# Optimization experiments

Hardware: AMD Instinct MI355X
Metric: run time of the kernel (lower is better)

The kernel has to match this reference:

```python
import jax, jax.numpy as jnp
import numpy as np

D_MODEL = 1024
NUM_HEADS = 16
WINDOW = 128
DEPTH = D_MODEL // NUM_HEADS


def setup_inputs() -> dict:
    key = jax.random.key(0)
    ks = jax.random.split(key, 9)
    B, S = 2, 2048
    scale = 1.0 / np.sqrt(D_MODEL)
    x = jax.random.normal(ks[0], (B, S, D_MODEL), dtype=jnp.float32)
    Wq = jax.random.normal(ks[1], (D_MODEL, D_MODEL), dtype=jnp.float32) * scale
    Wk = jax.random.normal(ks[2], (D_MODEL, D_MODEL), dtype=jnp.float32) * scale
    Wv = jax.random.normal(ks[3], (D_MODEL, D_MODEL), dtype=jnp.float32) * scale
    Wo = jax.random.normal(ks[4], (D_MODEL, D_MODEL), dtype=jnp.float32) * scale
    bq = jnp.zeros((D_MODEL,), jnp.float32)
    bk = jnp.zeros((D_MODEL,), jnp.float32)
    bv = jnp.zeros((D_MODEL,), jnp.float32)
    bo = jnp.zeros((D_MODEL,), jnp.float32)
    return {"x": x, "Wq": Wq, "bq": bq, "Wk": Wk, "bk": bk,
            "Wv": Wv, "bv": bv, "Wo": Wo, "bo": bo}


def _split_heads(t, B, S):
    # [B,S,D] -> [B,H,S,depth]
    return t.reshape(B, S, NUM_HEADS, DEPTH).transpose(0, 2, 1, 3)


def reference(x, Wq, bq, Wk, bk, Wv, bv, Wo, bo):
    B, S, _ = x.shape
    q = _split_heads(x @ Wq + bq, B, S)
    k = _split_heads(x @ Wk + bk, B, S)
    v = _split_heads(x @ Wv + bv, B, S)
    scores = jnp.einsum('bhqd,bhkd->bhqk', q, k) / jnp.sqrt(jnp.float32(DEPTH))
    idx = jnp.arange(S)
    # mask[i_row=j, i_col=i] per original: |i - j| <= window (symmetric)
    local = jnp.abs(idx[None, :] - idx[:, None]) <= WINDOW  # [S,S]
    scores = jnp.where(local[None, None], scores, jnp.float32(-1e9))
    attn = jax.nn.softmax(scores, axis=-1)
    out = jnp.einsum('bhqk,bhkd->bhqd', attn, v)
    concat = out.transpose(0, 2, 1, 3).reshape(B, S, D_MODEL)
    return concat @ Wo + bo
```

## Files before the change

### kernel.cpp

```cpp
#include <hip/hip_runtime.h>
#include <cstdint>
#include <cstddef>

typedef __attribute__((ext_vector_type(8))) short short8;
typedef __attribute__((ext_vector_type(4))) short short4v;
typedef __attribute__((ext_vector_type(4))) float f32x4;
typedef short8 bf16x8;

typedef __attribute__((address_space(1))) const unsigned GU;
typedef __attribute__((address_space(3))) unsigned LU;

__device__ __forceinline__ short f2bf(float f) {
  unsigned u = __builtin_bit_cast(unsigned, f);
  u += 0x7fffu + ((u >> 16) & 1u);
  return (short)(u >> 16);
}

__global__ __launch_bounds__(256) void k_cast_x(const float* __restrict__ x, short* __restrict__ xb) {
  size_t i = ((size_t)blockIdx.x * 256 + threadIdx.x) * 8;
  f32x4 a = *(const f32x4*)(x + i);
  f32x4 b = *(const f32x4*)(x + i + 4);
  short8 o;
#pragma unroll
  for (int j = 0; j < 4; ++j) { o[j] = f2bf(a[j]); o[4 + j] = f2bf(b[j]); }
  *(short8*)(xb + i) = o;
}

__global__ __launch_bounds__(256) void k_tw(const float* __restrict__ W0, const float* __restrict__ W1,
                                            const float* __restrict__ W2, const float* __restrict__ W3,
                                            short* __restrict__ WT) {
  __shared__ short T[64 * 72];
  int bid = blockIdx.x;
  int widx = bid >> 8;
  int t = bid & 255;
  int kr = (t >> 4) * 64, nc = (t & 15) * 64;
  const float* W = widx == 0 ? W0 : widx == 1 ? W1 : widx == 2 ? W2 : W3;
  short* out = WT + (size_t)widx * 1048576;
  int tid = threadIdx.x;
#pragma unroll
  for (int i = 0; i < 4; ++i) {
    int idx = tid + i * 256;
    int k = idx >> 4, n4 = (idx & 15) << 2;
    f32x4 v = *(const f32x4*)(W + (size_t)(kr + k) * 1024 + nc + n4);
#pragma unroll
    for (int j = 0; j < 4; ++j) T[(n4 + j) * 72 + k] = f2bf(v[j]);
  }
  __syncthreads();
#pragma unroll
  for (int i = 0; i < 2; ++i) {
    int idx = tid + i * 256;
    int n = idx >> 3, k8 = (idx & 7) << 3;
    *(short8*)(out + (size_t)(nc + n) * 1024 + kr + k8) = *(const short8*)&T[n * 72 + k8];
  }
}

__global__ __launch_bounds__(256) void k_tv(const short* __restrict__ v, short* __restrict__ vT) {
  __shared__ short T[64 * 72];
  int bid = blockIdx.x;
  int stile = bid & 31, h = (bid >> 5) & 15, b = bid >> 9;
  int s0 = stile * 64;
  int tid = threadIdx.x;
#pragma unroll
  for (int i = 0; i < 2; ++i) {
    int idx = tid + i * 256;
    int s = idx >> 3, d0 = (idx & 7) << 3;
    short8 vec = *(const short8*)(v + ((size_t)b * 2048 + s0 + s) * 1024 + h * 64 + d0);
#pragma unroll
    for (int j = 0; j < 8; ++j) T[(d0 + j) * 72 + s] = vec[j];
  }
  __syncthreads();
#pragma unroll
  for (int i = 0; i < 2; ++i) {
    int idx = tid + i * 256;
    int d = idx >> 3, s8 = (idx & 7) << 3;
    *(short8*)(vT + (((size_t)b * 16 + h) * 64 + d) * 2048 + s0 + s8) = *(const short8*)&T[d * 72 + s8];
  }
}

template <int MODE>
__global__ __launch_bounds__(256, 2) void k_gemm(
    const short* __restrict__ A, const short* __restrict__ BT,
    const float* __restrict__ bias0, const float* __restrict__ bias1, const float* __restrict__ bias2,
    short* __restrict__ outb, float* __restrict__ outf) {
  __shared__ short Smem[16384];
  const int tid = threadIdx.x;
  const int lane = tid & 63, w = tid >> 6;
  const int g = lane >> 4, qi = lane & 15;
  const int wr = (w >> 1) * 64, wc = (w & 1) * 64;
  const int m0 = blockIdx.y * 128, n0 = blockIdx.x * 128;
  const size_t K = 1024;
  const short* Ab = A + (size_t)m0 * K;
  const short* Bb = BT + (size_t)n0 * K;

  auto stage = [&](int buf, int k0) {
    short* Asb = Smem + buf * 4096;
    short* Bsb = Smem + 8192 + buf * 4096;
#pragma unroll
    for (int i = 0; i < 2; ++i) {
      int cidx = tid + i * 256;
      int r = cidx >> 2;
      int csw = ((cidx & 3) ^ ((r >> 1) & 3)) << 3;
      __builtin_amdgcn_global_load_lds((GU*)(Ab + (size_t)r * K + k0 + csw),
                                       (LU*)(&Asb[cidx * 8]), 16, 0, 0);
      __builtin_amdgcn_global_load_lds((GU*)(Bb + (size_t)r * K + k0 + csw),
                                       (LU*)(&Bsb[cidx * 8]), 16, 0, 0);
    }
  };

  f32x4 acc[4][4];
#pragma unroll
  for (int i = 0; i < 4; ++i)
#pragma unroll
    for (int j = 0; j < 4; ++j) acc[i][j] = (f32x4)(0.0f);

  stage(0, 0);
  __syncthreads();
  for (int kt = 0; kt < 32; ++kt) {
    int cur = kt & 1;
    if (kt < 31) stage(cur ^ 1, (kt + 1) * 32);
    const short* Asb = Smem + cur * 4096;
    const short* Bsb = Smem + 8192 + cur * 4096;
    bf16x8 a[4], b[4];
#pragma unroll
    for (int mf = 0; mf < 4; ++mf) {
      int R = wr + mf * 16 + qi;
      a[mf] = *(const bf16x8*)&Asb[R * 32 + ((g ^ ((R >> 1) & 3)) << 3)];
    }
#pragma unroll
    for (int nf = 0; nf < 4; ++nf) {
      int R = wc + nf * 16 + qi;
      b[nf] = *(const bf16x8*)&Bsb[R * 32 + ((g ^ ((R >> 1) & 3)) << 3)];
    }
#pragma unroll
    for (int mf = 0; mf < 4; ++mf)
#pragma unroll
      for (int nf = 0; nf < 4; ++nf)
        acc[mf][nf] = __builtin_amdgcn_mfma_f32_16x16x32_bf16(a[mf], b[nf], acc[mf][nf], 0, 0, 0);
    __syncthreads();
  }

  if (MODE == 0) {
    int sel = n0 >> 10;
    const float* bias = sel == 0 ? bias0 : (sel == 1 ? bias1 : bias2);
    size_t outoff = (size_t)sel * 4194304;
    int ncol0 = n0 & 1023;
    float bv[4];
#pragma unroll
    for (int nf = 0; nf < 4; ++nf) bv[nf] = bias[ncol0 + wc + nf * 16 + qi];
    short* Os = Smem;
#pragma unroll
    for (int mf = 0; mf < 4; ++mf) {
      __syncthreads();
#pragma unroll
      for (int nf = 0; nf < 4; ++nf)
#pragma unroll
        for (int j = 0; j < 4; ++j)
          Os[((w >> 1) * 16 + g * 4 + j) * 136 + wc + nf * 16 + qi] = f2bf(acc[mf][nf][j] + bv[nf]);
      __syncthreads();
#pragma unroll
      for (int i = 0; i < 2; ++i) {
        int idx = tid + i * 256;
        int r = idx >> 4, c8 = (idx & 15) << 3;
        int row = m0 + ((r >> 4) << 6) + mf * 16 + (r & 15);
        *(short8*)&outb[outoff + (size_t)row * 1024 + ncol0 + c8] = *(const short8*)&Os[r * 136 + c8];
      }
    }
  } else {
    float* Ft = (float*)Smem;
    float bv[4];
#pragma unroll
    for (int nf = 0; nf < 4; ++nf) bv[nf] = bias0[n0 + wc + nf * 16 + qi];
#pragma unroll
    for (int mf = 0; mf < 4; ++mf) {
      __syncthreads();
#pragma unroll
      for (int nf = 0; nf < 4; ++nf)
#pragma unroll
        for (int j = 0; j < 4; ++j)
          Ft[((w >> 1) * 16 + g * 4 + j) * 136 + wc + nf * 16 + qi] = acc[mf][nf][j] + bv[nf];
      __syncthreads();
#pragma unroll
      for (int i = 0; i < 4; ++i) {
        int idx = tid + i * 256;
        int r = idx >> 5, c4 = (idx & 31) << 2;
        int row = m0 + ((r >> 4) << 6) + mf * 16 + (r & 15);
        *(f32x4*)&outf[(size_t)row * 1024 + n0 + c4] = *(const f32x4*)&Ft[r * 136 + c4];
      }
    }
  }
}

__global__ __launch_bounds__(256, 2) void k_attn(const short* __restrict__ qg_,
                                                 const short* __restrict__ kg_,
                                                 const short* __restrict__ vT,
                                                 short* __restrict__ outp) {
  __shared__ short Qs[64 * 72];
  __shared__ short Ks[64 * 72];
  __shared__ short Vs[64 * 72];
  __shared__ short Ps[4][16 * 72];
  int bid = blockIdx.x;
  int qt = bid & 31, h = (bid >> 5) & 15, b = bid >> 9;
  int q0 = qt * 64;
  int tid = threadIdx.x, lane = tid & 63, w = tid >> 6;
  int g = lane >> 4, qi = lane & 15;

  const short* qsrc = qg_ + ((size_t)b * 2048 + q0) * 1024 + h * 64;
#pragma unroll
  for (int i = 0; i < 2; ++i) {
    int idx = tid + i * 256;
    int r = idx >> 3, c = (idx & 7) << 3;
    *(short8*)&Qs[r * 72 + c] = *(const short8*)&qsrc[(size_t)r * 1024 + c];
  }

  float m = -1e30f, l = 0.f;
  f32x4 oacc[4];
#pragma unroll
  for (int i = 0; i < 4; ++i) oacc[i] = (f32x4)(0.0f);
  int qglob = q0 + w * 16 + qi;

  for (int cc = 0; cc < 5; ++cc) {
    int kb0 = q0 - 128 + cc * 64;
    if (kb0 < 0 || kb0 >= 2048) continue;
    __syncthreads();
    const short* ksrc = kg_ + ((size_t)b * 2048 + kb0) * 1024 + h * 64;
    const short* vsrc = vT + ((size_t)(b * 16 + h)) * 64 * 2048 + kb0;
#pragma unroll
    for (int i = 0; i < 2; ++i) {
      int idx = tid + i * 256;
      int r = idx >> 3, c = (idx & 7) << 3;
      *(short8*)&Ks[r * 72 + c] = *(const short8*)&ksrc[(size_t)r * 1024 + c];
      *(short8*)&Vs[r * 72 + c] = *(const short8*)&vsrc[(size_t)r * 2048 + c];
    }
    __syncthreads();

    f32x4 st[4];
#pragma unroll
    for (int i = 0; i < 4; ++i) st[i] = (f32x4)(0.0f);
#pragma unroll
    for (int ds = 0; ds < 2; ++ds) {
      bf16x8 qf = *(const bf16x8*)&Qs[(w * 16 + qi) * 72 + ds * 32 + g * 8];
#pragma unroll
      for (int mf = 0; mf < 4; ++mf) {
        bf16x8 kf = *(const bf16x8*)&Ks[(mf * 16 + qi) * 72 + ds * 32 + g * 8];
        st[mf] = __builtin_amdgcn_mfma_f32_16x16x32_bf16(kf, qf, st[mf], 0, 0, 0);
      }
    }

    float pv[16];
    float pm = -1e30f;
#pragma unroll
    for (int mf = 0; mf < 4; ++mf)
#pragma unroll
      for (int j = 0; j < 4; ++j) {
        int kcol = kb0 + mf * 16 + g * 4 + j;
        float s = st[mf][j] * 0.125f;
        int d = kcol - qglob;
        bool valid = (d >= -128) && (d <= 128);
        s = valid ? s : -1e30f;
        pv[mf * 4 + j] = s;
        pm = fmaxf(pm, s);
      }
    pm = fmaxf(pm, __shfl_xor(pm, 16));
    pm = fmaxf(pm, __shfl_xor(pm, 32));
    float mnew = fmaxf(m, pm);
    float scale = __expf(m - mnew);
    float ls = 0.f;
#pragma unroll
    for (int e = 0; e < 16; ++e) {
      float p = pv[e] > -1e29f ? __expf(pv[e] - mnew) : 0.f;
      pv[e] = p;
      ls += p;
    }
    ls += __shfl_xor(ls, 16);
    ls += __shfl_xor(ls, 32);
    l = l * scale + ls;
    m = mnew;
#pragma unroll
    for (int mf = 0; mf < 4; ++mf) oacc[mf] *= scale;

#pragma unroll
    for (int f = 0; f < 4; ++f) {
      short4v pk;
#pragma unroll
      for (int j = 0; j < 4; ++j) pk[j] = f2bf(pv[f * 4 + j]);
      *(short4v*)&Ps[w][qi * 72 + f * 16 + g * 4] = pk;
    }

#pragma unroll
    for (int ks = 0; ks < 2; ++ks) {
      bf16x8 pf = *(const bf16x8*)&Ps[w][qi * 72 + ks * 32 + g * 8];
#pragma unroll
      for (int mf = 0; mf < 4; ++mf) {
        bf16x8 vf = *(const bf16x8*)&Vs[(mf * 16 + qi) * 72 + ks * 32 + g * 8];
        oacc[mf] = __builtin_amdgcn_mfma_f32_16x16x32_bf16(vf, pf, oacc[mf], 0, 0, 0);
      }
    }
  }

  __syncthreads();
  short* Os = Ks;
  float inv = 1.f / l;
#pragma unroll
  for (int mf = 0; mf < 4; ++mf) {
    short4v pk;
#pragma unroll
    for (int j = 0; j < 4; ++j) pk[j] = f2bf(oacc[mf][j] * inv);
    *(short4v*)&Os[(w * 16 + qi) * 72 + mf * 16 + g * 4] = pk;
  }
  __syncthreads();
  short* dst = outp + ((size_t)b * 2048 + q0) * 1024 + h * 64;
  int r = tid >> 2, c16 = (tid & 3) << 4;
  *(short8*)&dst[(size_t)r * 1024 + c16] = *(const short8*)&Os[r * 72 + c16];
  *(short8*)&dst[(size_t)r * 1024 + c16 + 8] = *(const short8*)&Os[r * 72 + c16 + 8];
}

extern "C" void kernel_launch(void* const* d_in, const int* in_sizes, int n_in,
                              void* d_out, int out_size, void* d_ws, size_t ws_size,
                              hipStream_t stream) {
  const float* x  = (const float*)d_in[0];
  const float* Wq = (const float*)d_in[1];
  const float* bq = (const float*)d_in[2];
  const float* Wk = (const float*)d_in[3];
  const float* bk = (const float*)d_in[4];
  const float* Wv = (const float*)d_in[5];
  const float* bv = (const float*)d_in[6];
  const float* Wo = (const float*)d_in[7];
  const float* bo = (const float*)d_in[8];

  short* ws = (short*)d_ws;
  short* xb       = ws;
  short* qkv      = ws + 4194304;
  short* vbuf     = qkv + 2 * 4194304;
  short* vT       = ws;
  short* attn_out = vbuf;
  short* WT       = ws + 4 * 4194304;

  k_cast_x<<<2048, 256, 0, stream>>>(x, xb);
  k_tw<<<1024, 256, 0, stream>>>(Wq, Wk, Wv, Wo, WT);
  {
    dim3 grid(24, 32);
    k_gemm<0><<<grid, 256, 0, stream>>>(xb, WT, bq, bk, bv, qkv, nullptr);
  }
  k_tv<<<1024, 256, 0, stream>>>(vbuf, vT);
  k_attn<<<1024, 256, 0, stream>>>(qkv, qkv + 4194304, vT, attn_out);
  {
    dim3 grid(8, 32);
    k_gemm<1><<<grid, 256, 0, stream>>>(attn_out, WT + 3 * 1048576, bo, bo, bo, nullptr, (float*)d_out);
  }
}
```

Measured before the change: 96.34 us.

## Replace QKV GEMM with 256x256-tile, 8-wave, multi-stage pipelined kernel

The fused QKV projection GEMM moves from 128x128 tiles with 4 waves to 256x256 tiles with 8 waves. Global-to-LDS loads are staged in half-k chunks across a 128KB LDS ring and interleaved with MFMA phases, using explicit barriers, waitcnt and setprio. A block-index swizzle is added to improve L2 reuse. The larger tile cuts operand reloads and is meant to hide memory latency, but the grid drops to 192 blocks on 256 CUs, so some CUs sit idle.

Result: faster. 92.98 us (-3.5%).

```diff
diff --git a/kernel.cpp b/kernel.cpp
--- a/kernel.cpp
+++ b/kernel.cpp
@@ -77,11 +77,134 @@
   }
 }
 
-template <int MODE>
-__global__ __launch_bounds__(256, 2) void k_gemm(
+__global__ __launch_bounds__(512, 2) void k_gemm256(
     const short* __restrict__ A, const short* __restrict__ BT,
     const float* __restrict__ bias0, const float* __restrict__ bias1, const float* __restrict__ bias2,
-    short* __restrict__ outb, float* __restrict__ outf) {
+    short* __restrict__ outb) {
+  __shared__ short S[65536];
+  const int tid = threadIdx.x;
+  const int lane = tid & 63, w = tid >> 6;
+  const int g = lane >> 4, qi = lane & 15;
+  const int wm = w >> 2, wn = w & 3;
+  int bid = blockIdx.x;
+  int swz = (bid & 7) * 24 + (bid >> 3);
+  const int tm = swz / 12, tn = swz % 12;
+  const int m0 = tm * 256, n0 = tn * 256;
+  const size_t K = 1024;
+  const short* Ab = A + (size_t)m0 * K;
+  const short* Bb = BT + (size_t)n0 * K;
+
+  auto stage = [&](int roff, const short* gbase, int kt, int kh) {
+    int k0 = kt * 64 + kh * 32;
+#pragma unroll
+    for (int i = 0; i < 2; ++i) {
+      int c = tid + i * 512;
+      int r = c >> 2;
+      int csw = ((c & 3) ^ ((r >> 1) & 3)) << 3;
+      __builtin_amdgcn_global_load_lds((GU*)(gbase + (size_t)r * K + k0 + csw),
+                                       (LU*)(&S[roff + c * 8]), 16, 0, 0);
+    }
+  };
+  auto lda = [&](int roff, int row) -> bf16x8 {
+    return *(const bf16x8*)&S[roff + row * 32 + ((g ^ ((row >> 1) & 3)) << 3)];
+  };
+
+  f32x4 acc[8][4];
+#pragma unroll
+  for (int i = 0; i < 8; ++i)
+#pragma unroll
+    for (int j = 0; j < 4; ++j) acc[i][j] = (f32x4)(0.0f);
+
+#define MF1(rh, mf, nf, av, bv) \
+  acc[(rh)*4+(mf)][(nf)] = __builtin_amdgcn_mfma_f32_16x16x32_bf16(av, bv, acc[(rh)*4+(mf)][(nf)], 0, 0, 0)
+
+#define GPH(buf, kh, rh, ...) do { \
+    const int ra_ = (buf)*32768 + (kh)*8192; \
+    const int rb_ = (buf)*32768 + 16384 + (kh)*8192; \
+    const int ar_ = wm*128 + (rh)*64 + qi; \
+    bf16x8 a0 = lda(ra_, ar_ + 0);  bf16x8 a1 = lda(ra_, ar_ + 16); \
+    bf16x8 a2 = lda(ra_, ar_ + 32); bf16x8 a3 = lda(ra_, ar_ + 48); \
+    const int br_ = wn*64 + qi; \
+    bf16x8 b0 = lda(rb_, br_ + 0);  bf16x8 b1 = lda(rb_, br_ + 16); \
+    bf16x8 b2 = lda(rb_, br_ + 32); bf16x8 b3 = lda(rb_, br_ + 48); \
+    __VA_ARGS__; \
+    __builtin_amdgcn_sched_barrier(0); \
+    __builtin_amdgcn_s_barrier(); \
+    asm volatile("s_waitcnt lgkmcnt(0)" ::: "memory"); \
+    __builtin_amdgcn_sched_barrier(0); \
+    __builtin_amdgcn_s_setprio(1); \
+    MF1(rh,0,0,a0,b0); MF1(rh,0,1,a0,b1); MF1(rh,0,2,a0,b2); MF1(rh,0,3,a0,b3); \
+    MF1(rh,1,0,a1,b0); MF1(rh,1,1,a1,b1); MF1(rh,1,2,a1,b2); MF1(rh,1,3,a1,b3); \
+    MF1(rh,2,0,a2,b0); MF1(rh,2,1,a2,b1); MF1(rh,2,2,a2,b2); MF1(rh,2,3,a2,b3); \
+    MF1(rh,3,0,a3,b0); MF1(rh,3,1,a3,b1); MF1(rh,3,2,a3,b2); MF1(rh,3,3,a3,b3); \
+    __builtin_amdgcn_s_setprio(0); \
+    __builtin_amdgcn_sched_barrier(0); \
+  } while (0)
+
+  stage(0,     Ab, 0, 0);
+  stage(16384, Bb, 0, 0);
+  stage(8192,  Ab, 0, 1);
+  stage(24576, Bb, 0, 1);
+  stage(32768, Ab, 1, 0);
+  stage(49152, Bb, 1, 0);
+  asm volatile("s_waitcnt vmcnt(4)" ::: "memory");
+  __builtin_amdgcn_s_barrier();
+
+  for (int j = 0; j < 8; ++j) {
+    int t1 = 2 * j + 1;
+    int t2 = 2 * j + 2; t2 = t2 < 15 ? t2 : 15;
+    int t3 = 2 * j + 3; t3 = t3 < 15 ? t3 : 15;
+    GPH(0, 0, 0, stage(40960, Ab, t1, 1));  __builtin_amdgcn_s_barrier();
+    GPH(0, 0, 1, stage(57344, Bb, t1, 1));  __builtin_amdgcn_s_barrier();
+    GPH(0, 1, 0, stage(0,     Ab, t2, 0));  __builtin_amdgcn_s_barrier();
+    GPH(0, 1, 1, stage(16384, Bb, t2, 0));
+      asm volatile("s_waitcnt vmcnt(4)" ::: "memory");
+      __builtin_amdgcn_s_barrier();
+    GPH(1, 0, 0, stage(8192,  Ab, t2, 1));  __builtin_amdgcn_s_barrier();
+    GPH(1, 0, 1, stage(24576, Bb, t2, 1));  __builtin_amdgcn_s_barrier();
+    GPH(1, 1, 0, stage(32768, Ab, t3, 0));  __builtin_amdgcn_s_barrier();
+    GPH(1, 1, 1, stage(49152, Bb, t3, 0));
+      asm volatile("s_waitcnt vmcnt(4)" ::: "memory");
+      __builtin_amdgcn_s_barrier();
+  }
+#undef GPH
+#undef MF1
+
+  asm volatile("s_waitcnt vmcnt(0)" ::: "memory");
+  __syncthreads();
+  int sel = n0 >> 10;
+  const float* bias = sel == 0 ? bias0 : (sel == 1 ? bias1 : bias2);
+  size_t outoff = (size_t)sel * 4194304;
+  int ncol0 = n0 & 1023;
+  float bv[4];
+#pragma unroll
+  for (int nf = 0; nf < 4; ++nf) bv[nf] = bias[ncol0 + wn * 64 + nf * 16 + qi];
+  short* Ep = S;
+#pragma unroll
+  for (int rh = 0; rh < 2; ++rh) {
+    __syncthreads();
+#pragma unroll
+    for (int mf = 0; mf < 4; ++mf)
+#pragma unroll
+      for (int nf = 0; nf < 4; ++nf)
+#pragma unroll
+        for (int j = 0; j < 4; ++j)
+          Ep[(wm * 64 + mf * 16 + g * 4 + j) * 264 + wn * 64 + nf * 16 + qi] =
+              f2bf(acc[rh * 4 + mf][nf][j] + bv[nf]);
+    __syncthreads();
+#pragma unroll
+    for (int i = 0; i < 8; ++i) {
+      int idx = tid + i * 512;
+      int r = idx >> 5, c8 = (idx & 31) << 3;
+      int grow = m0 + (r >> 6) * 128 + rh * 64 + (r & 63);
+      *(short8*)&outb[outoff + (size_t)grow * 1024 + ncol0 + c8] = *(const short8*)&Ep[r * 264 + c8];
+    }
+  }
+}
+
+__global__ __launch_bounds__(256, 2) void k_gemmO(
+    const short* __restrict__ A, const short* __restrict__ BT,
+    const float* __restrict__ bias0, float* __restrict__ outf) {
   __shared__ short Smem[16384];
   const int tid = threadIdx.x;
   const int lane = tid & 63, w = tid >> 6;
@@ -139,53 +262,25 @@
     __syncthreads();
   }
 
-  if (MODE == 0) {
-    int sel = n0 >> 10;
-    const float* bias = sel == 0 ? bias0 : (sel == 1 ? bias1 : bias2);
-    size_t outoff = (size_t)sel * 4194304;
-    int ncol0 = n0 & 1023;
-    float bv[4];
-#pragma unroll
-    for (int nf = 0; nf < 4; ++nf) bv[nf] = bias[ncol0 + wc + nf * 16 + qi];
-    short* Os = Smem;
-#pragma unroll
-    for (int mf = 0; mf < 4; ++mf) {
-      __syncthreads();
-#pragma unroll
-      for (int nf = 0; nf < 4; ++nf)
-#pragma unroll
-        for (int j = 0; j < 4; ++j)
-          Os[((w >> 1) * 16 + g * 4 + j) * 136 + wc + nf * 16 + qi] = f2bf(acc[mf][nf][j] + bv[nf]);
-      __syncthreads();
-#pragma unroll
-      for (int i = 0; i < 2; ++i) {
-        int idx = tid + i * 256;
-        int r = idx >> 4, c8 = (idx & 15) << 3;
-        int row = m0 + ((r >> 4) << 6) + mf * 16 + (r & 15);
-        *(short8*)&outb[outoff + (size_t)row * 1024 + ncol0 + c8] = *(const short8*)&Os[r * 136 + c8];
-      }
-    }
-  } else {
-    float* Ft = (float*)Smem;
-    float bv[4];
-#pragma unroll
-    for (int nf = 0; nf < 4; ++nf) bv[nf] = bias0[n0 + wc + nf * 16 + qi];
-#pragma unroll
-    for (int mf = 0; mf < 4; ++mf) {
-      __syncthreads();
-#pragma unroll
-      for (int nf = 0; nf < 4; ++nf)
-#pragma unroll
-        for (int j = 0; j < 4; ++j)
-          Ft[((w >> 1) * 16 + g * 4 + j) * 136 + wc + nf * 16 + qi] = acc[mf][nf][j] + bv[nf];
-      __syncthreads();
-#pragma unroll
-      for (int i = 0; i < 4; ++i) {
-        int idx = tid + i * 256;
-        int r = idx >> 5, c4 = (idx & 31) << 2;
-        int row = m0 + ((r >> 4) << 6) + mf * 16 + (r & 15);
-        *(f32x4*)&outf[(size_t)row * 1024 + n0 + c4] = *(const f32x4*)&Ft[r * 136 + c4];
-      }
+  float* Ft = (float*)Smem;
+  float bv[4];
+#pragma unroll
+  for (int nf = 0; nf < 4; ++nf) bv[nf] = bias0[n0 + wc + nf * 16 + qi];
+#pragma unroll
+  for (int mf = 0; mf < 4; ++mf) {
+    __syncthreads();
+#pragma unroll
+    for (int nf = 0; nf < 4; ++nf)
+#pragma unroll
+      for (int j = 0; j < 4; ++j)
+        Ft[((w >> 1) * 16 + g * 4 + j) * 136 + wc + nf * 16 + qi] = acc[mf][nf][j] + bv[nf];
+    __syncthreads();
+#pragma unroll
+    for (int i = 0; i < 4; ++i) {
+      int idx = tid + i * 256;
+      int r = idx >> 5, c4 = (idx & 31) << 2;
+      int row = m0 + ((r >> 4) << 6) + mf * 16 + (r & 15);
+      *(f32x4*)&outf[(size_t)row * 1024 + n0 + c4] = *(const f32x4*)&Ft[r * 136 + c4];
     }
   }
 }
@@ -337,14 +432,11 @@
 
   k_cast_x<<<2048, 256, 0, stream>>>(x, xb);
   k_tw<<<1024, 256, 0, stream>>>(Wq, Wk, Wv, Wo, WT);
-  {
-    dim3 grid(24, 32);
-    k_gemm<0><<<grid, 256, 0, stream>>>(xb, WT, bq, bk, bv, qkv, nullptr);
-  }
+  k_gemm256<<<192, 512, 0, stream>>>(xb, WT, bq, bk, bv, qkv);
   k_tv<<<1024, 256, 0, stream>>>(vbuf, vT);
   k_attn<<<1024, 256, 0, stream>>>(qkv, qkv + 4194304, vT, attn_out);
   {
     dim3 grid(8, 32);
-    k_gemm<1><<<grid, 256, 0, stream>>>(attn_out, WT + 3 * 1048576, bo, bo, bo, nullptr, (float*)d_out);
-  }
-}
+    k_gemmO<<<grid, 256, 0, stream>>>(attn_out, WT + 3 * 1048576, bo, (float*)d_out);
+  }
+}
```

## Merge prep kernels, drop V transpose kernel, remap QKV GEMM tiles per XCD

Applied to the files above, without the earlier changes.

Merges the x cast and weight transpose into one launch. Removes the separate V transpose kernel: attention now reads V in its original layout and transposes it into LDS with a rotated column swizzle, so the MFMA read side changes to match. The QKV GEMM becomes a 1D grid whose block index is remapped so each XCD works on a contiguous group of M and N tiles, aiming for better L2 reuse. Together these cut two launches and one full pass over V through global memory, at the cost of scalar LDS stores of V inside attention.

Result: faster. 86.35 us (-10.4%).

```diff
diff --git a/kernel.cpp b/kernel.cpp
--- a/kernel.cpp
+++ b/kernel.cpp
@@ -16,27 +16,29 @@
   return (short)(u >> 16);
 }
 
-__global__ __launch_bounds__(256) void k_cast_x(const float* __restrict__ x, short* __restrict__ xb) {
-  size_t i = ((size_t)blockIdx.x * 256 + threadIdx.x) * 8;
-  f32x4 a = *(const f32x4*)(x + i);
-  f32x4 b = *(const f32x4*)(x + i + 4);
-  short8 o;
-#pragma unroll
-  for (int j = 0; j < 4; ++j) { o[j] = f2bf(a[j]); o[4 + j] = f2bf(b[j]); }
-  *(short8*)(xb + i) = o;
-}
-
-__global__ __launch_bounds__(256) void k_tw(const float* __restrict__ W0, const float* __restrict__ W1,
-                                            const float* __restrict__ W2, const float* __restrict__ W3,
-                                            short* __restrict__ WT) {
+__global__ __launch_bounds__(256) void k_prep(const float* __restrict__ x,
+                                              const float* __restrict__ W0, const float* __restrict__ W1,
+                                              const float* __restrict__ W2, const float* __restrict__ W3,
+                                              short* __restrict__ xb, short* __restrict__ WT) {
   __shared__ short T[64 * 72];
   int bid = blockIdx.x;
+  int tid = threadIdx.x;
+  if (bid < 2048) {
+    size_t i = ((size_t)bid * 256 + tid) * 8;
+    f32x4 a = *(const f32x4*)(x + i);
+    f32x4 b = *(const f32x4*)(x + i + 4);
+    short8 o;
+#pragma unroll
+    for (int j = 0; j < 4; ++j) { o[j] = f2bf(a[j]); o[4 + j] = f2bf(b[j]); }
+    *(short8*)(xb + i) = o;
+    return;
+  }
+  bid -= 2048;
   int widx = bid >> 8;
   int t = bid & 255;
   int kr = (t >> 4) * 64, nc = (t & 15) * 64;
   const float* W = widx == 0 ? W0 : widx == 1 ? W1 : widx == 2 ? W2 : W3;
   short* out = WT + (size_t)widx * 1048576;
-  int tid = threadIdx.x;
 #pragma unroll
   for (int i = 0; i < 4; ++i) {
     int idx = tid + i * 256;
@@ -54,34 +56,101 @@
   }
 }
 
-__global__ __launch_bounds__(256) void k_tv(const short* __restrict__ v, short* __restrict__ vT) {
-  __shared__ short T[64 * 72];
-  int bid = blockIdx.x;
-  int stile = bid & 31, h = (bid >> 5) & 15, b = bid >> 9;
-  int s0 = stile * 64;
-  int tid = threadIdx.x;
-#pragma unroll
-  for (int i = 0; i < 2; ++i) {
-    int idx = tid + i * 256;
-    int s = idx >> 3, d0 = (idx & 7) << 3;
-    short8 vec = *(const short8*)(v + ((size_t)b * 2048 + s0 + s) * 1024 + h * 64 + d0);
-#pragma unroll
-    for (int j = 0; j < 8; ++j) T[(d0 + j) * 72 + s] = vec[j];
-  }
-  __syncthreads();
-#pragma unroll
-  for (int i = 0; i < 2; ++i) {
-    int idx = tid + i * 256;
-    int d = idx >> 3, s8 = (idx & 7) << 3;
-    *(short8*)(vT + (((size_t)b * 16 + h) * 64 + d) * 2048 + s0 + s8) = *(const short8*)&T[d * 72 + s8];
-  }
-}
-
-template <int MODE>
-__global__ __launch_bounds__(256, 2) void k_gemm(
+__global__ __launch_bounds__(256, 2) void k_gemmQKV(
     const short* __restrict__ A, const short* __restrict__ BT,
     const float* __restrict__ bias0, const float* __restrict__ bias1, const float* __restrict__ bias2,
-    short* __restrict__ outb, float* __restrict__ outf) {
+    short* __restrict__ outb) {
+  __shared__ short Smem[16384];
+  const int tid = threadIdx.x;
+  const int lane = tid & 63, w = tid >> 6;
+  const int g = lane >> 4, qi = lane & 15;
+  const int wr = (w >> 1) * 64, wc = (w & 1) * 64;
+  int bid = blockIdx.x;
+  int xcd = bid & 7, ii = bid >> 3;
+  const int tm = (xcd >> 1) * 8 + ii / 12;
+  const int tn = (xcd & 1) * 12 + ii % 12;
+  const int m0 = tm * 128, n0 = tn * 128;
+  const size_t K = 1024;
+  const short* Ab = A + (size_t)m0 * K;
+  const short* Bb = BT + (size_t)n0 * K;
+
+  auto stage = [&](int buf, int k0) {
+    short* Asb = Smem + buf * 4096;
+    short* Bsb = Smem + 8192 + buf * 4096;
+#pragma unroll
+    for (int i = 0; i < 2; ++i) {
+      int cidx = tid + i * 256;
+      int r = cidx >> 2;
+      int csw = ((cidx & 3) ^ ((r >> 1) & 3)) << 3;
+      __builtin_amdgcn_global_load_lds((GU*)(Ab + (size_t)r * K + k0 + csw),
+                                       (LU*)(&Asb[cidx * 8]), 16, 0, 0);
+      __builtin_amdgcn_global_load_lds((GU*)(Bb + (size_t)r * K + k0 + csw),
+                                       (LU*)(&Bsb[cidx * 8]), 16, 0, 0);
+    }
+  };
+
+  f32x4 acc[4][4];
+#pragma unroll
+  for (int i = 0; i < 4; ++i)
+#pragma unroll
+    for (int j = 0; j < 4; ++j) acc[i][j] = (f32x4)(0.0f);
+
+  stage(0, 0);
+  __syncthreads();
+  for (int kt = 0; kt < 32; ++kt) {
+    int cur = kt & 1;
+    if (kt < 31) stage(cur ^ 1, (kt + 1) * 32);
+    const short* Asb = Smem + cur * 4096;
+    const short* Bsb = Smem + 8192 + cur * 4096;
+    bf16x8 a[4], b[4];
+#pragma unroll
+    for (int mf = 0; mf < 4; ++mf) {
+      int R = wr + mf * 16 + qi;
+      a[mf] = *(const bf16x8*)&Asb[R * 32 + ((g ^ ((R >> 1) & 3)) << 3)];
+    }
+#pragma unroll
+    for (int nf = 0; nf < 4; ++nf) {
+      int R = wc + nf * 16 + qi;
+      b[nf] = *(const bf16x8*)&Bsb[R * 32 + ((g ^ ((R >> 1) & 3)) << 3)];
+    }
+#pragma unroll
+    for (int mf = 0; mf < 4; ++mf)
+#pragma unroll
+      for (int nf = 0; nf < 4; ++nf)
+        acc[mf][nf] = __builtin_amdgcn_mfma_f32_16x16x32_bf16(a[mf], b[nf], acc[mf][nf], 0, 0, 0);
+    __syncthreads();
+  }
+
+  int sel = n0 >> 10;
+  const float* bias = sel == 0 ? bias0 : (sel == 1 ? bias1 : bias2);
+  size_t outoff = (size_t)sel * 4194304;
+  int ncol0 = n0 & 1023;
+  float bv[4];
+#pragma unroll
+  for (int nf = 0; nf < 4; ++nf) bv[nf] = bias[ncol0 + wc + nf * 16 + qi];
+  short* Os = Smem;
+#pragma unroll
+  for (int mf = 0; mf < 4; ++mf) {
+    __syncthreads();
+#pragma unroll
+    for (int nf = 0; nf < 4; ++nf)
+#pragma unroll
+      for (int j = 0; j < 4; ++j)
+        Os[((w >> 1) * 16 + g * 4 + j) * 136 + wc + nf * 16 + qi] = f2bf(acc[mf][nf][j] + bv[nf]);
+    __syncthreads();
+#pragma unroll
+    for (int i = 0; i < 2; ++i) {
+      int idx = tid + i * 256;
+      int r = idx >> 4, c8 = (idx & 15) << 3;
+      int row = m0 + ((r >> 4) << 6) + mf * 16 + (r & 15);
+      *(short8*)&outb[outoff + (size_t)row * 1024 + ncol0 + c8] = *(const short8*)&Os[r * 136 + c8];
+    }
+  }
+}
+
+__global__ __launch_bounds__(256, 2) void k_gemmO(
+    const short* __restrict__ A, const short* __restrict__ BT,
+    const float* __restrict__ bias0, float* __restrict__ outf) {
   __shared__ short Smem[16384];
   const int tid = threadIdx.x;
   const int lane = tid & 63, w = tid >> 6;
@@ -139,60 +208,32 @@
     __syncthreads();
   }
 
-  if (MODE == 0) {
-    int sel = n0 >> 10;
-    const float* bias = sel == 0 ? bias0 : (sel == 1 ? bias1 : bias2);
-    size_t outoff = (size_t)sel * 4194304;
-    int ncol0 = n0 & 1023;
-    float bv[4];
-#pragma unroll
-    for (int nf = 0; nf < 4; ++nf) bv[nf] = bias[ncol0 + wc + nf * 16 + qi];
-    short* Os = Smem;
-#pragma unroll
-    for (int mf = 0; mf < 4; ++mf) {
-      __syncthreads();
-#pragma unroll
-      for (int nf = 0; nf < 4; ++nf)
-#pragma unroll
-        for (int j = 0; j < 4; ++j)
-          Os[((w >> 1) * 16 + g * 4 + j) * 136 + wc + nf * 16 + qi] = f2bf(acc[mf][nf][j] + bv[nf]);
-      __syncthreads();
-#pragma unroll
-      for (int i = 0; i < 2; ++i) {
-        int idx = tid + i * 256;
-        int r = idx >> 4, c8 = (idx & 15) << 3;
-        int row = m0 + ((r >> 4) << 6) + mf * 16 + (r & 15);
-        *(short8*)&outb[outoff + (size_t)row * 1024 + ncol0 + c8] = *(const short8*)&Os[r * 136 + c8];
-      }
-    }
-  } else {
-    float* Ft = (float*)Smem;
-    float bv[4];
-#pragma unroll
-    for (int nf = 0; nf < 4; ++nf) bv[nf] = bias0[n0 + wc + nf * 16 + qi];
-#pragma unroll
-    for (int mf = 0; mf < 4; ++mf) {
-      __syncthreads();
-#pragma unroll
-      for (int nf = 0; nf < 4; ++nf)
-#pragma unroll
-        for (int j = 0; j < 4; ++j)
-          Ft[((w >> 1) * 16 + g * 4 + j) * 136 + wc + nf * 16 + qi] = acc[mf][nf][j] + bv[nf];
-      __syncthreads();
-#pragma unroll
-      for (int i = 0; i < 4; ++i) {
-        int idx = tid + i * 256;
-        int r = idx >> 5, c4 = (idx & 31) << 2;
-        int row = m0 + ((r >> 4) << 6) + mf * 16 + (r & 15);
-        *(f32x4*)&outf[(size_t)row * 1024 + n0 + c4] = *(const f32x4*)&Ft[r * 136 + c4];
-      }
+  float* Ft = (float*)Smem;
+  float bv[4];
+#pragma unroll
+  for (int nf = 0; nf < 4; ++nf) bv[nf] = bias0[n0 + wc + nf * 16 + qi];
+#pragma unroll
+  for (int mf = 0; mf < 4; ++mf) {
+    __syncthreads();
+#pragma unroll
+    for (int nf = 0; nf < 4; ++nf)
+#pragma unroll
+      for (int j = 0; j < 4; ++j)
+        Ft[((w >> 1) * 16 + g * 4 + j) * 136 + wc + nf * 16 + qi] = acc[mf][nf][j] + bv[nf];
+    __syncthreads();
+#pragma unroll
+    for (int i = 0; i < 4; ++i) {
+      int idx = tid + i * 256;
+      int r = idx >> 5, c4 = (idx & 31) << 2;
+      int row = m0 + ((r >> 4) << 6) + mf * 16 + (r & 15);
+      *(f32x4*)&outf[(size_t)row * 1024 + n0 + c4] = *(const f32x4*)&Ft[r * 136 + c4];
     }
   }
 }
 
 __global__ __launch_bounds__(256, 2) void k_attn(const short* __restrict__ qg_,
                                                  const short* __restrict__ kg_,
-                                                 const short* __restrict__ vT,
+                                                 const short* __restrict__ vg_,
                                                  short* __restrict__ outp) {
   __shared__ short Qs[64 * 72];
   __shared__ short Ks[64 * 72];
@@ -223,13 +264,18 @@
     if (kb0 < 0 || kb0 >= 2048) continue;
     __syncthreads();
     const short* ksrc = kg_ + ((size_t)b * 2048 + kb0) * 1024 + h * 64;
-    const short* vsrc = vT + ((size_t)(b * 16 + h)) * 64 * 2048 + kb0;
+    const short* vsrc = vg_ + ((size_t)b * 2048 + kb0) * 1024 + h * 64;
 #pragma unroll
     for (int i = 0; i < 2; ++i) {
       int idx = tid + i * 256;
       int r = idx >> 3, c = (idx & 7) << 3;
       *(short8*)&Ks[r * 72 + c] = *(const short8*)&ksrc[(size_t)r * 1024 + c];
-      *(short8*)&Vs[r * 72 + c] = *(const short8*)&vsrc[(size_t)r * 2048 + c];
+      short8 vv = *(const short8*)&vsrc[(size_t)r * 1024 + c];
+#pragma unroll
+      for (int j = 0; j < 8; ++j) {
+        int d = c + j;
+        Vs[d * 72 + ((r + ((d >> 3) << 3)) & 63)] = vv[j];
+      }
     }
     __syncthreads();
 
@@ -291,7 +337,9 @@
       bf16x8 pf = *(const bf16x8*)&Ps[w][qi * 72 + ks * 32 + g * 8];
 #pragma unroll
       for (int mf = 0; mf < 4; ++mf) {
-        bf16x8 vf = *(const bf16x8*)&Vs[(mf * 16 + qi) * 72 + ks * 32 + g * 8];
+        int dd = mf * 16 + qi;
+        int pc = ((ks * 32 + g * 8) + ((dd >> 3) << 3)) & 63;
+        bf16x8 vf = *(const bf16x8*)&Vs[dd * 72 + pc];
         oacc[mf] = __builtin_amdgcn_mfma_f32_16x16x32_bf16(vf, pf, oacc[mf], 0, 0, 0);
       }
     }
@@ -331,20 +379,14 @@
   short* xb       = ws;
   short* qkv      = ws + 4194304;
   short* vbuf     = qkv + 2 * 4194304;
-  short* vT       = ws;
-  short* attn_out = vbuf;
+  short* attn_out = ws;
   short* WT       = ws + 4 * 4194304;
 
-  k_cast_x<<<2048, 256, 0, stream>>>(x, xb);
-  k_tw<<<1024, 256, 0, stream>>>(Wq, Wk, Wv, Wo, WT);
-  {
-    dim3 grid(24, 32);
-    k_gemm<0><<<grid, 256, 0, stream>>>(xb, WT, bq, bk, bv, qkv, nullptr);
-  }
-  k_tv<<<1024, 256, 0, stream>>>(vbuf, vT);
-  k_attn<<<1024, 256, 0, stream>>>(qkv, qkv + 4194304, vT, attn_out);
+  k_prep<<<3072, 256, 0, stream>>>(x, Wq, Wk, Wv, Wo, xb, WT);
+  k_gemmQKV<<<768, 256, 0, stream>>>(xb, WT, bq, bk, bv, qkv);
+  k_attn<<<1024, 256, 0, stream>>>(qkv, qkv + 4194304, vbuf, attn_out);
   {
     dim3 grid(8, 32);
-    k_gemm<1><<<grid, 256, 0, stream>>>(attn_out, WT + 3 * 1048576, bo, bo, bo, nullptr, (float*)d_out);
-  }
-}
+    k_gemmO<<<grid, 256, 0, stream>>>(attn_out, WT + 3 * 1048576, bo, (float*)d_out);
+  }
+}
```
